# Kernel tuning notes

Hardware: AMD Instinct MI355X
Metric: run time of the kernel (lower is better)

Reference implementation:

```python
import jax, jax.numpy as jnp
import numpy as np

D_STATE = 16
DT_RANK = 4


def selective_scan(u, delta, A, Bc, Cc, D):
    """Mamba selective scan.
    u, delta: [S, L, d]; A: [d, N]; Bc, Cc: [S, L, N]; D: [d].
    Returns y: [S, L, d].
    """
    # discretize: deltaA [S,L,d,N], deltaB*u [S,L,d,N]
    dA = jnp.exp(delta[..., None] * A)
    dBu = (delta * u)[..., None] * Bc[:, :, None, :]

    def step(h, inp):
        dA_t, dBu_t, C_t = inp  # [S,d,N], [S,d,N], [S,N]
        h = dA_t * h + dBu_t
        y = jnp.einsum('sdn,sn->sd', h, C_t)
        return h, y

    S, L, d = u.shape
    N = A.shape[1]
    h0 = jnp.zeros((S, d, N), u.dtype)
    _, ys = jax.lax.scan(
        step, h0,
        (dA.transpose(1, 0, 2, 3), dBu.transpose(1, 0, 2, 3), Cc.transpose(1, 0, 2)))
    y = ys.transpose(1, 0, 2)  # [S, L, d]
    return y + u * D


def ssm_branch(u, A_log, D, x_proj_w, dt_proj_w, dt_proj_b):
    """u: [S, L, d] sequence of tokens; applies input-dependent SSM."""
    N = A_log.shape[1]
    proj = jnp.einsum('sld,pd->slp', u, x_proj_w)  # [S,L,dt_rank+2N]
    dt_raw = proj[..., :DT_RANK]
    Bc = proj[..., DT_RANK:DT_RANK + N]
    Cc = proj[..., DT_RANK + N:]
    delta = jax.nn.softplus(jnp.einsum('slr,dr->sld', dt_raw, dt_proj_w) + dt_proj_b)
    A = -jnp.exp(A_log)  # [d, N]
    return selective_scan(u, delta, A, Bc, Cc, D)


def setup_inputs() -> dict:
    key = jax.random.key(0)
    ks = jax.random.split(key, 6)
    B, C, H, W = 4, 64, 128, 128
    x = jax.random.normal(ks[0], (B, C, H, W), jnp.float32)
    A_log = jnp.log(jax.random.uniform(ks[1], (C, D_STATE), jnp.float32, 0.5, 4.0))
    D = jax.random.normal(ks[2], (C,), jnp.float32)
    x_proj_w = jax.random.normal(ks[3], (DT_RANK + 2 * D_STATE, C), jnp.float32) * (C ** -0.5)
    dt_proj_w = jax.random.normal(ks[4], (C, DT_RANK), jnp.float32) * (DT_RANK ** -0.5)
    dt_proj_b = jax.random.normal(ks[5], (C,), jnp.float32) * 0.1
    return {"x": x, "A_log": A_log, "D": D, "x_proj_w": x_proj_w,
            "dt_proj_w": dt_proj_w, "dt_proj_b": dt_proj_b}


def reference(x, A_log, D, x_proj_w, dt_proj_w, dt_proj_b):
    B, C, H, W = x.shape
    # horizontal scan: B*H row-sequences of length W
    u_h = x.transpose(0, 2, 3, 1).reshape(B * H, W, C)
    y_h = ssm_branch(u_h, A_log, D, x_proj_w, dt_proj_w, dt_proj_b)
    y_h = y_h.reshape(B, H, W, C).transpose(0, 3, 1, 2)
    # vertical scan: B*W column-sequences of length H
    u_v = x.transpose(0, 3, 2, 1).reshape(B * W, H, C)
    y_v = ssm_branch(u_v, A_log, D, x_proj_w, dt_proj_w, dt_proj_b)
    y_v = y_v.reshape(B, W, H, C).transpose(0, 3, 2, 1)
    return y_h + y_v
```

## Files before the change

kernel.cpp:

```cpp
#include <hip/hip_runtime.h>

#define BB 4
#define CC 64
#define HH 128
#define WW 128
#define NN 16
#define HW (HH*WW)

__device__ __forceinline__ float softplus_f(float x) {
    float e = __expf(-fabsf(x));
    return fmaxf(x, 0.0f) + __logf(1.0f + e);
}

__global__ __launch_bounds__(256) void k_scan(
    const float* __restrict__ x, const float* __restrict__ xpw,
    const float* __restrict__ A_log, const float* __restrict__ Dv,
    const float* __restrict__ dtw, const float* __restrict__ dtb,
    float* __restrict__ out, float* __restrict__ yv)
{
    __shared__ float xt[128 * 64];
    __shared__ float bcs[128 * 32];
    __shared__ float dtr[128 * 4];
    __shared__ float dlt[8 * 64];

    const int t = threadIdx.x;
    const int half = blockIdx.x >> 9;
    const int r9 = blockIdx.x & 511;
    const int b = r9 >> 7;
    const int L = r9 & 127;

    if (half == 0) {
#pragma unroll
        for (int k = 0; k < 8; ++k) {
            int i = k * 256 + t;
            int c = i >> 5, jq = i & 31;
            float4 v = *(const float4*)&x[((size_t)(b * CC + c) * HH + L) * WW + jq * 4];
            int j0 = jq * 4;
            xt[(j0 + 0) * 64 + ((c + j0 + 0) & 63)] = v.x;
            xt[(j0 + 1) * 64 + ((c + j0 + 1) & 63)] = v.y;
            xt[(j0 + 2) * 64 + ((c + j0 + 2) & 63)] = v.z;
            xt[(j0 + 3) * 64 + ((c + j0 + 3) & 63)] = v.w;
        }
    } else {
#pragma unroll
        for (int p = 0; p < 32; ++p) {
            int c = t & 63, j = p * 4 + (t >> 6);
            xt[j * 64 + ((c + j) & 63)] =
                x[((size_t)(b * CC + c) * HH + j) * WW + L];
        }
    }
    __syncthreads();

    {
        const int wv = t >> 6, lane = t & 63;
        const int pg2 = __builtin_amdgcn_readfirstlane(wv & 1);
        const int pix = (wv >> 1) * 64 + lane;
        const int p0 = pg2 * 18;
        const int sw = pix & 7;
        float acc[18];
#pragma unroll
        for (int j = 0; j < 18; ++j) acc[j] = 0.f;
        for (int c4 = 0; c4 < 16; ++c4) {
            float xv0 = xt[pix * 64 + ((c4 * 4 + 0 + pix) & 63)];
            float xv1 = xt[pix * 64 + ((c4 * 4 + 1 + pix) & 63)];
            float xv2 = xt[pix * 64 + ((c4 * 4 + 2 + pix) & 63)];
            float xv3 = xt[pix * 64 + ((c4 * 4 + 3 + pix) & 63)];
#pragma unroll
            for (int j = 0; j < 18; ++j) {
                float4 wq = *(const float4*)&xpw[(p0 + j) * CC + c4 * 4];
                acc[j] = fmaf(wq.x, xv0, fmaf(wq.y, xv1,
                         fmaf(wq.z, xv2, fmaf(wq.w, xv3, acc[j]))));
            }
        }
        float* bp = &bcs[pix * 32];
        if (pg2 == 0) {
            *(float4*)&dtr[pix * 4] = make_float4(acc[0], acc[1], acc[2], acc[3]);
            *(float4*)&bp[((0 ^ sw) << 2)] = make_float4(acc[4], acc[5], acc[6], acc[7]);
            *(float4*)&bp[((1 ^ sw) << 2)] = make_float4(acc[8], acc[9], acc[10], acc[11]);
            *(float4*)&bp[((2 ^ sw) << 2)] = make_float4(acc[12], acc[13], acc[14], acc[15]);
            bp[((3 ^ sw) << 2) + 0] = acc[16];
            bp[((3 ^ sw) << 2) + 1] = acc[17];
        } else {
            bp[((3 ^ sw) << 2) + 2] = acc[0];
            bp[((3 ^ sw) << 2) + 3] = acc[1];
            *(float4*)&bp[((4 ^ sw) << 2)] = make_float4(acc[2], acc[3], acc[4], acc[5]);
            *(float4*)&bp[((5 ^ sw) << 2)] = make_float4(acc[6], acc[7], acc[8], acc[9]);
            *(float4*)&bp[((6 ^ sw) << 2)] = make_float4(acc[10], acc[11], acc[12], acc[13]);
            *(float4*)&bp[((7 ^ sw) << 2)] = make_float4(acc[14], acc[15], acc[16], acc[17]);
        }
    }

    const int d = t >> 2, ng = t & 3, n0 = ng * 4;
    float A0 = -__expf(A_log[d * NN + n0 + 0]);
    float A1 = -__expf(A_log[d * NN + n0 + 1]);
    float A2 = -__expf(A_log[d * NN + n0 + 2]);
    float A3 = -__expf(A_log[d * NN + n0 + 3]);
    const float Dd = Dv[d];
    float h0 = 0.f, h1 = 0.f, h2 = 0.f, h3 = 0.f;
    const int dd = t & 63, jb = t >> 6;
    const float4 wt4 = *(const float4*)&dtw[dd * 4];
    const float bdd = dtb[dd];
    float* drow = (half == 0 ? out : yv) + ((size_t)(b * CC + d) * 128 + L) * 128;

    for (int ch = 0; ch < 16; ++ch) {
        __syncthreads();
#pragma unroll
        for (int k = 0; k < 2; ++k) {
            int jl = jb * 2 + k;
            float4 dr = *(const float4*)&dtr[(ch * 8 + jl) * 4];
            float draw = fmaf(dr.x, wt4.x, fmaf(dr.y, wt4.y,
                         fmaf(dr.z, wt4.z, fmaf(dr.w, wt4.w, bdd))));
            dlt[jl * 64 + dd] = softplus_f(draw);
        }
        __syncthreads();
        float y0 = 0.f, y1 = 0.f;
#pragma unroll
        for (int jl = 0; jl < 8; ++jl) {
            const int j = ch * 8 + jl;
            float delta = dlt[jl * 64 + d];
            float u = xt[j * 64 + ((d + j) & 63)];
            const int s = j & 7;
            float4 Bv = *(const float4*)&bcs[j * 32 + ((ng ^ s) << 2)];
            float4 Cv = *(const float4*)&bcs[j * 32 + (((4 + ng) ^ s) << 2)];
            float du = delta * u;
            h0 = fmaf(__expf(delta * A0), h0, du * Bv.x);
            h1 = fmaf(__expf(delta * A1), h1, du * Bv.y);
            h2 = fmaf(__expf(delta * A2), h2, du * Bv.z);
            h3 = fmaf(__expf(delta * A3), h3, du * Bv.w);
            float y = fmaf(h0, Cv.x, fmaf(h1, Cv.y, fmaf(h2, Cv.z, h3 * Cv.w)));
            y += __shfl_xor(y, 1);
            y += __shfl_xor(y, 2);
            y = fmaf(u, Dd, y);
            if (ng == (jl >> 1)) { if (jl & 1) y1 = y; else y0 = y; }
        }
        *(float2*)&drow[ch * 8 + ng * 2] = make_float2(y0, y1);
    }
}

__global__ __launch_bounds__(256) void k_add(const float* __restrict__ yv,
                                             float* __restrict__ out)
{
    __shared__ float td[32 * 33];
    int t = threadIdx.x;
    int bc_ = blockIdx.x >> 4;
    int tb = blockIdx.x & 15;
    int w0 = (tb & 3) * 32;
    int h0 = (tb >> 2) * 32;
    const float* src = yv + (size_t)bc_ * HW;
    float* dst = out + (size_t)bc_ * HW;
    int r = t >> 3, q = t & 7;
    float4 v = *(const float4*)&src[(w0 + r) * HH + h0 + q * 4];
    td[r * 33 + q * 4 + 0] = v.x;
    td[r * 33 + q * 4 + 1] = v.y;
    td[r * 33 + q * 4 + 2] = v.z;
    td[r * 33 + q * 4 + 3] = v.w;
    __syncthreads();
    float* op = &dst[(h0 + r) * WW + w0 + q * 4];
    float4 o = *(float4*)op;
    o.x += td[(q * 4 + 0) * 33 + r];
    o.y += td[(q * 4 + 1) * 33 + r];
    o.z += td[(q * 4 + 2) * 33 + r];
    o.w += td[(q * 4 + 3) * 33 + r];
    *(float4*)op = o;
}

extern "C" void kernel_launch(void* const* d_in, const int* in_sizes, int n_in,
                              void* d_out, int out_size, void* d_ws, size_t ws_size,
                              hipStream_t stream) {
    const float* x     = (const float*)d_in[0];
    const float* A_log = (const float*)d_in[1];
    const float* Dv    = (const float*)d_in[2];
    const float* xpw   = (const float*)d_in[3];
    const float* dtw   = (const float*)d_in[4];
    const float* dtb   = (const float*)d_in[5];
    float* out = (float*)d_out;
    float* yv  = (float*)d_ws;

    k_scan<<<1024, 256, 0, stream>>>(x, xpw, A_log, Dv, dtw, dtb, out, yv);
    k_add <<<BB * CC * 16, 256, 0, stream>>>(yv, out);
}
```

Baseline: 152.0 us.

## Split scan into two 64-step segments and compute delta in-quad with DPP broadcast

The kernel now processes each 128-long sequence in two 64-element segments, halving shared memory (xt/bcs/dtr). That raises possible occupancy, and the projection is split across all four waves with 9 outputs each instead of 18. The per-chunk delta shared buffer and its two barriers per chunk are removed. Each quad lane computes softplus deltas for two timesteps and broadcasts them with DPP quad_perm. This adds one extra barrier per segment and somewhat redundant softplus work per quad.

```diff
diff --git a/kernel.cpp b/kernel.cpp
--- a/kernel.cpp
+++ b/kernel.cpp
@@ -12,128 +12,144 @@
     return fmaxf(x, 0.0f) + __logf(1.0f + e);
 }
 
+template<int SRC>
+__device__ __forceinline__ float quad_bcast(float v) {
+    return __int_as_float(__builtin_amdgcn_mov_dpp(
+        __float_as_int(v), SRC * 0x55, 0xF, 0xF, true));
+}
+
 __global__ __launch_bounds__(256) void k_scan(
     const float* __restrict__ x, const float* __restrict__ xpw,
     const float* __restrict__ A_log, const float* __restrict__ Dv,
     const float* __restrict__ dtw, const float* __restrict__ dtb,
     float* __restrict__ out, float* __restrict__ yv)
 {
-    __shared__ float xt[128 * 64];
-    __shared__ float bcs[128 * 32];
-    __shared__ float dtr[128 * 4];
-    __shared__ float dlt[8 * 64];
+    __shared__ float xt[64 * 64];
+    __shared__ float bcs[64 * 32];
+    __shared__ float dtr[64 * 4];
 
     const int t = threadIdx.x;
     const int half = blockIdx.x >> 9;
     const int r9 = blockIdx.x & 511;
     const int b = r9 >> 7;
     const int L = r9 & 127;
+    const int wv = t >> 6, lane = t & 63;
 
-    if (half == 0) {
+    const int d = t >> 2, ng = t & 3, n0 = ng * 4;
+    const float A0 = -__expf(A_log[d * NN + n0 + 0]);
+    const float A1 = -__expf(A_log[d * NN + n0 + 1]);
+    const float A2 = -__expf(A_log[d * NN + n0 + 2]);
+    const float A3 = -__expf(A_log[d * NN + n0 + 3]);
+    const float Dd = Dv[d];
+    const float4 wt4 = *(const float4*)&dtw[d * 4];
+    const float bdd = dtb[d];
+    float h0 = 0.f, h1 = 0.f, h2 = 0.f, h3 = 0.f;
+    float* drow = (half == 0 ? out : yv) + ((size_t)(b * CC + d) * 128 + L) * 128;
+
+    const int p0 = __builtin_amdgcn_readfirstlane(wv * 9);
+
+    for (int seg = 0; seg < 2; ++seg) {
+        if (seg) __syncthreads();
+
+        if (half == 0) {
 #pragma unroll
-        for (int k = 0; k < 8; ++k) {
-            int i = k * 256 + t;
-            int c = i >> 5, jq = i & 31;
-            float4 v = *(const float4*)&x[((size_t)(b * CC + c) * HH + L) * WW + jq * 4];
-            int j0 = jq * 4;
-            xt[(j0 + 0) * 64 + ((c + j0 + 0) & 63)] = v.x;
-            xt[(j0 + 1) * 64 + ((c + j0 + 1) & 63)] = v.y;
-            xt[(j0 + 2) * 64 + ((c + j0 + 2) & 63)] = v.z;
-            xt[(j0 + 3) * 64 + ((c + j0 + 3) & 63)] = v.w;
-        }
-    } else {
+            for (int k = 0; k < 4; ++k) {
+                int i = k * 256 + t;
+                int c = i >> 4, j0 = (i & 15) * 4;
+                float4 v = *(const float4*)&x[((size_t)(b * CC + c) * HH + L) * WW
+                                              + seg * 64 + j0];
+                xt[(j0 + 0) * 64 + ((c + j0 + 0) & 63)] = v.x;
+                xt[(j0 + 1) * 64 + ((c + j0 + 1) & 63)] = v.y;
+                xt[(j0 + 2) * 64 + ((c + j0 + 2) & 63)] = v.z;
+                xt[(j0 + 3) * 64 + ((c + j0 + 3) & 63)] = v.w;
+            }
+        } else {
 #pragma unroll
-        for (int p = 0; p < 32; ++p) {
-            int c = t & 63, j = p * 4 + (t >> 6);
-            xt[j * 64 + ((c + j) & 63)] =
-                x[((size_t)(b * CC + c) * HH + j) * WW + L];
-        }
-    }
-    __syncthreads();
-
-    {
-        const int wv = t >> 6, lane = t & 63;
-        const int pg2 = __builtin_amdgcn_readfirstlane(wv & 1);
-        const int pix = (wv >> 1) * 64 + lane;
-        const int p0 = pg2 * 18;
-        const int sw = pix & 7;
-        float acc[18];
-#pragma unroll
-        for (int j = 0; j < 18; ++j) acc[j] = 0.f;
-        for (int c4 = 0; c4 < 16; ++c4) {
-            float xv0 = xt[pix * 64 + ((c4 * 4 + 0 + pix) & 63)];
-            float xv1 = xt[pix * 64 + ((c4 * 4 + 1 + pix) & 63)];
-            float xv2 = xt[pix * 64 + ((c4 * 4 + 2 + pix) & 63)];
-            float xv3 = xt[pix * 64 + ((c4 * 4 + 3 + pix) & 63)];
-#pragma unroll
-            for (int j = 0; j < 18; ++j) {
-                float4 wq = *(const float4*)&xpw[(p0 + j) * CC + c4 * 4];
-                acc[j] = fmaf(wq.x, xv0, fmaf(wq.y, xv1,
-                         fmaf(wq.z, xv2, fmaf(wq.w, xv3, acc[j]))));
+            for (int p = 0; p < 16; ++p) {
+                int jl = p * 4 + wv;
+                xt[jl * 64 + ((lane + jl) & 63)] =
+                    x[((size_t)(b * CC + lane) * HH + seg * 64 + jl) * WW + L];
             }
         }
-        float* bp = &bcs[pix * 32];
-        if (pg2 == 0) {
-            *(float4*)&dtr[pix * 4] = make_float4(acc[0], acc[1], acc[2], acc[3]);
-            *(float4*)&bp[((0 ^ sw) << 2)] = make_float4(acc[4], acc[5], acc[6], acc[7]);
-            *(float4*)&bp[((1 ^ sw) << 2)] = make_float4(acc[8], acc[9], acc[10], acc[11]);
-            *(float4*)&bp[((2 ^ sw) << 2)] = make_float4(acc[12], acc[13], acc[14], acc[15]);
-            bp[((3 ^ sw) << 2) + 0] = acc[16];
-            bp[((3 ^ sw) << 2) + 1] = acc[17];
-        } else {
-            bp[((3 ^ sw) << 2) + 2] = acc[0];
-            bp[((3 ^ sw) << 2) + 3] = acc[1];
-            *(float4*)&bp[((4 ^ sw) << 2)] = make_float4(acc[2], acc[3], acc[4], acc[5]);
-            *(float4*)&bp[((5 ^ sw) << 2)] = make_float4(acc[6], acc[7], acc[8], acc[9]);
-            *(float4*)&bp[((6 ^ sw) << 2)] = make_float4(acc[10], acc[11], acc[12], acc[13]);
-            *(float4*)&bp[((7 ^ sw) << 2)] = make_float4(acc[14], acc[15], acc[16], acc[17]);
-        }
-    }
+        __syncthreads();
 
-    const int d = t >> 2, ng = t & 3, n0 = ng * 4;
-    float A0 = -__expf(A_log[d * NN + n0 + 0]);
-    float A1 = -__expf(A_log[d * NN + n0 + 1]);
-    float A2 = -__expf(A_log[d * NN + n0 + 2]);
-    float A3 = -__expf(A_log[d * NN + n0 + 3]);
-    const float Dd = Dv[d];
-    float h0 = 0.f, h1 = 0.f, h2 = 0.f, h3 = 0.f;
-    const int dd = t & 63, jb = t >> 6;
-    const float4 wt4 = *(const float4*)&dtw[dd * 4];
-    const float bdd = dtb[dd];
-    float* drow = (half == 0 ? out : yv) + ((size_t)(b * CC + d) * 128 + L) * 128;
-
-    for (int ch = 0; ch < 16; ++ch) {
-        __syncthreads();
+        {
+            const int pix = lane, sw = pix & 7;
+            const float* xw = xpw + p0 * CC;
+            float acc[9];
 #pragma unroll
-        for (int k = 0; k < 2; ++k) {
-            int jl = jb * 2 + k;
-            float4 dr = *(const float4*)&dtr[(ch * 8 + jl) * 4];
-            float draw = fmaf(dr.x, wt4.x, fmaf(dr.y, wt4.y,
-                         fmaf(dr.z, wt4.z, fmaf(dr.w, wt4.w, bdd))));
-            dlt[jl * 64 + dd] = softplus_f(draw);
+            for (int j = 0; j < 9; ++j) acc[j] = 0.f;
+            for (int c4 = 0; c4 < 16; ++c4) {
+                float xv0 = xt[pix * 64 + ((c4 * 4 + 0 + pix) & 63)];
+                float xv1 = xt[pix * 64 + ((c4 * 4 + 1 + pix) & 63)];
+                float xv2 = xt[pix * 64 + ((c4 * 4 + 2 + pix) & 63)];
+                float xv3 = xt[pix * 64 + ((c4 * 4 + 3 + pix) & 63)];
+#pragma unroll
+                for (int j = 0; j < 9; ++j) {
+                    float4 wq = *(const float4*)&xw[j * CC + c4 * 4];
+                    acc[j] = fmaf(wq.x, xv0, fmaf(wq.y, xv1,
+                             fmaf(wq.z, xv2, fmaf(wq.w, xv3, acc[j]))));
+                }
+            }
+            float* bp = &bcs[pix * 32];
+            if (wv == 0) {
+                *(float4*)&dtr[pix * 4] = make_float4(acc[0], acc[1], acc[2], acc[3]);
+                *(float4*)&bp[((0 ^ sw) << 2)] = make_float4(acc[4], acc[5], acc[6], acc[7]);
+                bp[((1 ^ sw) << 2) + 0] = acc[8];
+            } else if (wv == 1) {
+                bp[((1 ^ sw) << 2) + 1] = acc[0];
+                bp[((1 ^ sw) << 2) + 2] = acc[1];
+                bp[((1 ^ sw) << 2) + 3] = acc[2];
+                *(float4*)&bp[((2 ^ sw) << 2)] = make_float4(acc[3], acc[4], acc[5], acc[6]);
+                bp[((3 ^ sw) << 2) + 0] = acc[7];
+                bp[((3 ^ sw) << 2) + 1] = acc[8];
+            } else if (wv == 2) {
+                bp[((3 ^ sw) << 2) + 2] = acc[0];
+                bp[((3 ^ sw) << 2) + 3] = acc[1];
+                *(float4*)&bp[((4 ^ sw) << 2)] = make_float4(acc[2], acc[3], acc[4], acc[5]);
+                bp[((5 ^ sw) << 2) + 0] = acc[6];
+                bp[((5 ^ sw) << 2) + 1] = acc[7];
+                bp[((5 ^ sw) << 2) + 2] = acc[8];
+            } else {
+                bp[((5 ^ sw) << 2) + 3] = acc[0];
+                *(float4*)&bp[((6 ^ sw) << 2)] = make_float4(acc[1], acc[2], acc[3], acc[4]);
+                *(float4*)&bp[((7 ^ sw) << 2)] = make_float4(acc[5], acc[6], acc[7], acc[8]);
+            }
         }
         __syncthreads();
-        float y0 = 0.f, y1 = 0.f;
-#pragma unroll
-        for (int jl = 0; jl < 8; ++jl) {
-            const int j = ch * 8 + jl;
-            float delta = dlt[jl * 64 + d];
-            float u = xt[j * 64 + ((d + j) & 63)];
-            const int s = j & 7;
-            float4 Bv = *(const float4*)&bcs[j * 32 + ((ng ^ s) << 2)];
-            float4 Cv = *(const float4*)&bcs[j * 32 + (((4 + ng) ^ s) << 2)];
-            float du = delta * u;
-            h0 = fmaf(__expf(delta * A0), h0, du * Bv.x);
-            h1 = fmaf(__expf(delta * A1), h1, du * Bv.y);
-            h2 = fmaf(__expf(delta * A2), h2, du * Bv.z);
-            h3 = fmaf(__expf(delta * A3), h3, du * Bv.w);
-            float y = fmaf(h0, Cv.x, fmaf(h1, Cv.y, fmaf(h2, Cv.z, h3 * Cv.w)));
-            y += __shfl_xor(y, 1);
-            y += __shfl_xor(y, 2);
-            y = fmaf(u, Dd, y);
-            if (ng == (jl >> 1)) { if (jl & 1) y1 = y; else y0 = y; }
+
+#define SCAN_STEP(JL, DSRC)                                                    \
+        {                                                                      \
+            float delta = quad_bcast<(JL) & 3>(DSRC);                          \
+            const int jj = ch * 8 + (JL);                                      \
+            float u = xt[jj * 64 + ((d + jj) & 63)];                           \
+            float4 Bv = *(const float4*)&bcs[jj * 32 + ((ng ^ (JL)) << 2)];    \
+            float4 Cv = *(const float4*)&bcs[jj * 32 + (((4 + ng) ^ (JL)) << 2)]; \
+            float du = delta * u;                                              \
+            h0 = fmaf(__expf(delta * A0), h0, du * Bv.x);                      \
+            h1 = fmaf(__expf(delta * A1), h1, du * Bv.y);                      \
+            h2 = fmaf(__expf(delta * A2), h2, du * Bv.z);                      \
+            h3 = fmaf(__expf(delta * A3), h3, du * Bv.w);                      \
+            float y = fmaf(h0, Cv.x, fmaf(h1, Cv.y, fmaf(h2, Cv.z, h3 * Cv.w))); \
+            y += __shfl_xor(y, 1);                                             \
+            y += __shfl_xor(y, 2);                                             \
+            y = fmaf(u, Dd, y);                                                \
+            if (ng == ((JL) >> 1)) { if ((JL) & 1) y1 = y; else y0 = y; }      \
         }
-        *(float2*)&drow[ch * 8 + ng * 2] = make_float2(y0, y1);
+
+        for (int ch = 0; ch < 8; ++ch) {
+            float4 drA = *(const float4*)&dtr[(ch * 8 + ng) * 4];
+            float4 drB = *(const float4*)&dtr[(ch * 8 + 4 + ng) * 4];
+            float da = softplus_f(fmaf(drA.x, wt4.x, fmaf(drA.y, wt4.y,
+                       fmaf(drA.z, wt4.z, fmaf(drA.w, wt4.w, bdd)))));
+            float db = softplus_f(fmaf(drB.x, wt4.x, fmaf(drB.y, wt4.y,
+                       fmaf(drB.z, wt4.z, fmaf(drB.w, wt4.w, bdd)))));
+            float y0 = 0.f, y1 = 0.f;
+            SCAN_STEP(0, da) SCAN_STEP(1, da) SCAN_STEP(2, da) SCAN_STEP(3, da)
+            SCAN_STEP(4, db) SCAN_STEP(5, db) SCAN_STEP(6, db) SCAN_STEP(7, db)
+            *(float2*)&drow[seg * 64 + ch * 8 + ng * 2] = make_float2(y0, y1);
+        }
+#undef SCAN_STEP
     }
 }
 
```

Result: slower. 207.8 us (+36.7%).
